# Kernel optimization log

Hardware: AMD Instinct MI355X
Metric: run time of the kernel (lower is better)

Reference implementation:

```python
import jax, jax.numpy as jnp
import numpy as np

LAMBDA_DEPTHG = 0.3
STEGO_TEMPERATURE = 0.1
KNN_K = 7
DEPTH_SIGMA = 0.5
EPS = 1e-8


def _l2norm(x):
    return x / jnp.sqrt(jnp.sum(x * x, axis=-1, keepdims=True) + EPS)


def _stego_loss(codes, feats, temperature, knn_k):
    # Pairwise cosine similarity of DINO features -> KNN graph (includes self).
    f = _l2norm(feats)                                  # (B,N,Df)
    sim_f = jnp.einsum('bnd,bmd->bnm', f, f)            # (B,N,N)
    _, knn_idx = jax.lax.top_k(sim_f, knn_k)            # (B,N,k) int32
    # Temperature-scaled InfoNCE over code similarities; KNN entries are positives.
    c = _l2norm(codes)                                  # (B,N,Dc)
    logits = jnp.einsum('bnd,bmd->bnm', c, c) / temperature  # (B,N,N)
    logp = jax.nn.log_softmax(logits, axis=-1)          # (B,N,N)
    pos_logp = jnp.take_along_axis(logp, knn_idx, axis=-1)   # (B,N,k)
    return -jnp.mean(pos_logp)


def _depth_guided_correlation_loss(codes, depth, sigma_d):
    # Gaussian depth affinity: pixels at similar depth should have similar codes.
    dd = depth[:, :, None] - depth[:, None, :]          # (B,N,N)
    w = jnp.exp(-(dd * dd) / (2.0 * sigma_d * sigma_d)) # (B,N,N)
    c = _l2norm(codes)
    s = jnp.einsum('bnd,bmd->bnm', c, c)                # (B,N,N) cosine corr
    return jnp.mean(w * (1.0 - s))


def setup_inputs() -> dict:
    key = jax.random.key(0)
    k1, k2, k3 = jax.random.split(key, 3)
    B, N = 2, 4096
    semantic_codes = jax.random.normal(k1, (B, N, 90), dtype=jnp.float32)
    dino_features = jax.random.normal(k2, (B, N, 384), dtype=jnp.float32)
    depth = jax.random.uniform(k3, (B, N), dtype=jnp.float32)
    return {"semantic_codes": semantic_codes, "dino_features": dino_features, "depth": depth}


def reference(semantic_codes, dino_features, depth):
    l_stego = _stego_loss(semantic_codes, dino_features, STEGO_TEMPERATURE, KNN_K)
    l_depthg = _depth_guided_correlation_loss(semantic_codes, depth, DEPTH_SIGMA)
    total = l_stego + LAMBDA_DEPTHG * l_depthg
    return (l_stego, l_depthg, total)
```

## Files before the change

kernel.cpp:

```cpp
#include <hip/hip_runtime.h>
#include <math.h>

#define NPTS 4096

typedef __attribute__((ext_vector_type(8))) short bf16x8;
typedef __attribute__((ext_vector_type(16))) float f32x16;
typedef long fp8x8;

#define KEEP(x) asm volatile("" : "+v"(x))

__device__ __forceinline__ f32x16 zero16() {
  f32x16 z;
#pragma unroll
  for (int i = 0; i < 16; ++i) z[i] = 0.f;
  return z;
}

__device__ __forceinline__ unsigned packkey(float x, int m) {
  unsigned u = __float_as_uint(x);
  unsigned key = u ^ ((unsigned)((int)u >> 31) | 0x80000000u);
  return (key & 0xFFFFF000u) | (unsigned)m;
}

__device__ __forceinline__ void cas7(unsigned v, unsigned* s) {
#pragma unroll
  for (int t = 0; t < 7; ++t) {
    const unsigned hi = s[t] >= v ? s[t] : v;
    const unsigned lo = s[t] >= v ? v : s[t];
    s[t] = hi;
    v = lo;
  }
}

#define KSENT 0u

__device__ __forceinline__ unsigned bf16pack(float a, float b) {
  unsigned ua = __float_as_uint(a); ua = (ua + 0x7FFFu + ((ua >> 16) & 1u)) >> 16;
  unsigned ub = __float_as_uint(b); ub = (ub + 0x7FFFu + ((ub >> 16) & 1u)) >> 16;
  return ua | (ub << 16);
}

__global__ __launch_bounds__(64) void norm_f(const float* __restrict__ feats,
                                             unsigned char* __restrict__ Fsw8) {
  const int row = blockIdx.x;
  const int lane = threadIdx.x;
  const int b = row >> 12, mt = (row >> 5) & 127, rl = row & 31;

  const float* f = feats + (size_t)row * 384;
  float v[8];
  float ss = 0.f;
  if (lane < 48) {
    float4 p0 = *(const float4*)(f + lane * 8);
    float4 p1 = *(const float4*)(f + lane * 8 + 4);
    v[0] = p0.x; v[1] = p0.y; v[2] = p0.z; v[3] = p0.w;
    v[4] = p1.x; v[5] = p1.y; v[6] = p1.z; v[7] = p1.w;
#pragma unroll
    for (int e = 0; e < 8; ++e) ss = fmaf(v[e], v[e], ss);
  }
#pragma unroll
  for (int m = 1; m <= 32; m <<= 1) ss += __shfl_xor(ss, m, 64);
  const float s8 = rsqrtf(ss + 1e-8f) * 8.0f;
  if (lane < 48) {
    int w0 = __builtin_amdgcn_cvt_pk_fp8_f32(v[0] * s8, v[1] * s8, 0, 0);
    w0 = __builtin_amdgcn_cvt_pk_fp8_f32(v[2] * s8, v[3] * s8, w0, 1);
    int w1 = __builtin_amdgcn_cvt_pk_fp8_f32(v[4] * s8, v[5] * s8, 0, 0);
    w1 = __builtin_amdgcn_cvt_pk_fp8_f32(v[6] * s8, v[7] * s8, w1, 1);
    const int kc = lane >> 1, hs = lane & 1;
    uint2 o = make_uint2((unsigned)w0, (unsigned)w1);
    *(uint2*)(Fsw8 + (((size_t)(b * 128 + mt) * 24 + kc) << 9) + (hs * 32 + rl) * 8) = o;
  }
}

__global__ __launch_bounds__(64) void norm_c(const float* __restrict__ codes,
                                             unsigned short* __restrict__ Csw,
                                             float* __restrict__ invc) {
  const int row = blockIdx.x;
  const int lane = threadIdx.x;
  const int b = row >> 12, mt = (row >> 5) & 127, rl = row & 31;

  const float* c = codes + (size_t)row * 90;
  float cv[8];
#pragma unroll
  for (int e = 0; e < 8; ++e) cv[e] = 0.f;
  if (lane < 11) {
    float4 p0 = *(const float4*)(c + lane * 8);
    float4 p1 = *(const float4*)(c + lane * 8 + 4);
    cv[0] = p0.x; cv[1] = p0.y; cv[2] = p0.z; cv[3] = p0.w;
    cv[4] = p1.x; cv[5] = p1.y; cv[6] = p1.z; cv[7] = p1.w;
  } else if (lane == 11) {
    cv[0] = c[88]; cv[1] = c[89];
  }
  float cs = 0.f;
#pragma unroll
  for (int e = 0; e < 8; ++e) cs = fmaf(cv[e], cv[e], cs);
#pragma unroll
  for (int m = 1; m <= 32; m <<= 1) cs += __shfl_xor(cs, m, 64);
  const float cinv = rsqrtf(cs + 1e-8f);
  if (lane < 12) {
    uint4 o;
    o.x = bf16pack(cv[0] * cinv, cv[1] * cinv);
    o.y = bf16pack(cv[2] * cinv, cv[3] * cinv);
    o.z = bf16pack(cv[4] * cinv, cv[5] * cinv);
    o.w = bf16pack(cv[6] * cinv, cv[7] * cinv);
    const int kc = lane >> 1, hs = lane & 1;
    *(uint4*)(Csw + (((size_t)(b * 128 + mt) * 6 + kc) << 9) + (hs * 32 + rl) * 8) = o;
  }
  if (lane == 0) invc[row] = cinv;
}

__global__ __launch_bounds__(256, 1) void knn_mfma(const unsigned char* __restrict__ Fsw8,
                                                   unsigned* __restrict__ cand) {
  __shared__ unsigned ckey[4][32][7];
  const int g = blockIdx.x;
  const int b = g & 1;
  const int p = (g >> 1) & 3;
  const int qt = g >> 3;
  const int q0 = qt * 32;
  const int tid = threadIdx.x;
  const int w = tid >> 6;
  const int lane = tid & 63;
  const int lo = lane & 31, hi4 = (lane >> 5) * 4;
  const unsigned char* Fb = Fsw8 + (size_t)b * 128 * 24 * 512;

  fp8x8 bfr[24];
  {
    const unsigned char* qb = Fb + ((size_t)qt * 24) * 512 + lane * 8;
#pragma unroll
    for (int t = 0; t < 24; ++t) bfr[t] = *(const fp8x8*)(qb + t * 512);
#pragma unroll
    for (int t = 0; t < 24; ++t) KEEP(bfr[t]);
  }
  unsigned s7[7];
#pragma unroll
  for (int t = 0; t < 7; ++t) s7[t] = KSENT;

  const int t0 = p * 32 + w * 8;
  const unsigned char* ab = Fb + ((size_t)t0 * 24) * 512 + lane * 8;

  fp8x8 a0[12], a1[12];
#pragma unroll
  for (int t = 0; t < 12; ++t) a0[t] = *(const fp8x8*)(ab + t * 512);
#pragma unroll
  for (int t = 0; t < 12; ++t) KEEP(a0[t]);

  for (int mt = 0; mt < 8; ++mt) {
    const unsigned char* art = ab + (size_t)mt * 24 * 512;
#pragma unroll
    for (int t = 0; t < 12; ++t) a1[t] = *(const fp8x8*)(art + (12 + t) * 512);
#pragma unroll
    for (int t = 0; t < 12; ++t) KEEP(a1[t]);
    f32x16 acc = zero16();
#pragma unroll
    for (int t = 0; t < 12; ++t)
      acc = __builtin_amdgcn_mfma_f32_32x32x16_fp8_fp8(a0[t], bfr[t], acc, 0, 0, 0);
    if (mt + 1 < 8) {
      const unsigned char* arn = ab + (size_t)(mt + 1) * 24 * 512;
#pragma unroll
      for (int t = 0; t < 12; ++t) a0[t] = *(const fp8x8*)(arn + t * 512);
#pragma unroll
      for (int t = 0; t < 12; ++t) KEEP(a0[t]);
    }
#pragma unroll
    for (int t = 0; t < 12; ++t)
      acc = __builtin_amdgcn_mfma_f32_32x32x16_fp8_fp8(a1[t], bfr[12 + t], acc, 0, 0, 0);
    const int mb = (t0 + mt) * 32 + hi4;
#pragma unroll
    for (int r = 0; r < 16; ++r) {
      const int m = mb + (r & 3) + 8 * (r >> 2);
      cas7(packkey(acc[r], m), s7);
    }
  }

#pragma unroll
  for (int t = 0; t < 7; ++t) {
    const unsigned ov = (unsigned)__shfl_xor((int)s7[t], 32, 64);
    cas7(ov, s7);
  }
  if (lane < 32) {
#pragma unroll
    for (int t = 0; t < 7; ++t) ckey[w][lo][t] = s7[t];
  }
  __syncthreads();

  if (tid < 32) {
    unsigned fs[7];
#pragma unroll
    for (int t = 0; t < 7; ++t) fs[t] = KSENT;
    for (int w2 = 0; w2 < 4; ++w2)
#pragma unroll
      for (int t = 0; t < 7; ++t) cas7(ckey[w2][tid][t], fs);
    unsigned* o = cand + ((size_t)((p * 2 + b) * NPTS) + q0 + tid) * 7;
#pragma unroll
    for (int t = 0; t < 7; ++t) o[t] = fs[t];
  }
}

__global__ __launch_bounds__(512, 1) void lse_depth(const unsigned short* __restrict__ Csw,
                                                    const float* __restrict__ depth,
                                                    float* __restrict__ slse_part,
                                                    float* __restrict__ dpart) {
  __shared__ float lsep[8][32];
  __shared__ float depp[8];
  const int g = blockIdx.x;
  const int b = g & 1;
  const int h = (g >> 1) & 1;
  const int qt = g >> 2;
  const int q0 = qt * 32;
  const int tid = threadIdx.x;
  const int w = tid >> 6;
  const int lane = tid & 63;
  const int lo = lane & 31, hi4 = (lane >> 5) * 4;
  const unsigned short* Cb = Csw + (size_t)b * 128 * 6 * 512;
  const float* db = depth + b * NPTS;

  bf16x8 bfr[6];
  {
    const unsigned short* qb = Cb + ((size_t)qt * 6) * 512 + lane * 8;
#pragma unroll
    for (int t = 0; t < 6; ++t) bfr[t] = *(const bf16x8*)(qb + t * 512);
#pragma unroll
    for (int t = 0; t < 6; ++t) KEEP(bfr[t]);
  }
  const float dq = db[q0 + lo];
  float slse = 0.f, sdep = 0.f;

  const int t0 = h * 64 + w * 8;
  const unsigned short* ab = Cb + ((size_t)t0 * 6) * 512 + lane * 8;

  bf16x8 a0[6], a1[6];
#pragma unroll
  for (int t = 0; t < 6; ++t) a0[t] = *(const bf16x8*)(ab + t * 512);
#pragma unroll
  for (int t = 0; t < 6; ++t) KEEP(a0[t]);

#define PROC3(A, GT)                                                           \
  {                                                                            \
    f32x16 acc = zero16();                                                     \
    _Pragma("unroll")                                                          \
    for (int t = 0; t < 6; ++t)                                                \
      acc = __builtin_amdgcn_mfma_f32_32x32x16_bf16(A[t], bfr[t], acc, 0, 0, 0); \
    float dvv[16];                                                             \
    _Pragma("unroll")                                                          \
    for (int k = 0; k < 4; ++k) {                                              \
      float4 dv = *(const float4*)(db + (GT) * 32 + hi4 + 8 * k);              \
      dvv[k * 4 + 0] = dv.x; dvv[k * 4 + 1] = dv.y;                            \
      dvv[k * 4 + 2] = dv.z; dvv[k * 4 + 3] = dv.w;                            \
    }                                                                          \
    _Pragma("unroll")                                                          \
    for (int r = 0; r < 16; ++r) {                                             \
      const float s = acc[r];                                                  \
      const float dd = dq - dvv[r];                                            \
      sdep += __expf(-2.f * dd * dd) * (1.f - s);                              \
      slse += __expf(fmaf(s, 10.f, -10.f));                                    \
    }                                                                          \
  }

  for (int mt = 0; mt < 8; mt += 2) {
    {
      const unsigned short* ar = ab + (size_t)(mt + 1) * 6 * 512;
#pragma unroll
      for (int t = 0; t < 6; ++t) a1[t] = *(const bf16x8*)(ar + t * 512);
#pragma unroll
      for (int t = 0; t < 6; ++t) KEEP(a1[t]);
    }
    PROC3(a0, t0 + mt)
    if (mt + 2 < 8) {
      const unsigned short* ar = ab + (size_t)(mt + 2) * 6 * 512;
#pragma unroll
      for (int t = 0; t < 6; ++t) a0[t] = *(const bf16x8*)(ar + t * 512);
#pragma unroll
      for (int t = 0; t < 6; ++t) KEEP(a0[t]);
    }
    PROC3(a1, t0 + mt + 1)
  }
#undef PROC3

  slse += __shfl_xor(slse, 32, 64);
  if (lane < 32) lsep[w][lo] = slse;
#pragma unroll
  for (int m = 1; m <= 32; m <<= 1) sdep += __shfl_xor(sdep, m, 64);
  if (lane == 0) depp[w] = sdep;
  __syncthreads();
  if (tid < 32) {
    float tot = 0.f;
#pragma unroll
    for (int w2 = 0; w2 < 8; ++w2) tot += lsep[w2][tid];
    slse_part[(size_t)((h * 2 + b) * NPTS) + q0 + tid] = tot;
  }
  if (tid == 32) {
    float d = 0.f;
#pragma unroll
    for (int w2 = 0; w2 < 8; ++w2) d += depp[w2];
    dpart[g] = d;
  }
}

__global__ __launch_bounds__(64) void gather_pos(const float* __restrict__ codes,
                                                 const float* __restrict__ invc,
                                                 const unsigned* __restrict__ cand,
                                                 float* __restrict__ gpart) {
  const int n = blockIdx.x;
  const int b = n >> 12, q = n & 4095;
  const int lane = threadIdx.x;

  unsigned s[7];
#pragma unroll
  for (int t = 0; t < 7; ++t) s[t] = KSENT;
#pragma unroll
  for (int pp = 0; pp < 4; ++pp) {
    const unsigned* cp = cand + ((size_t)((pp * 2 + b) * NPTS) + q) * 7;
#pragma unroll
    for (int t = 0; t < 7; ++t) cas7(cp[t], s);
  }
  bool has = false;
#pragma unroll
  for (int t = 0; t < 7; ++t) has = has || ((s[t] & 4095u) == (unsigned)q);
  if (!has) s[6] = (unsigned)q;

  const float* cn = codes + (size_t)n * 90;
  float2 a = make_float2(0.f, 0.f);
  if (lane < 45) a = *(const float2*)(cn + lane * 2);
  const float inva = invc[n];
  float ssum = 0.f;
#pragma unroll
  for (int k = 0; k < 7; ++k) {
    const int m = (int)(s[k] & 4095u);
    const float* cm = codes + ((size_t)(b << 12) + m) * 90;
    float2 bb = make_float2(0.f, 0.f);
    if (lane < 45) bb = *(const float2*)(cm + lane * 2);
    float p = fmaf(a.x, bb.x, a.y * bb.y);
#pragma unroll
    for (int w = 1; w <= 32; w <<= 1) p += __shfl_xor(p, w, 64);
    ssum += p * inva * invc[(b << 12) + m];
  }
  if (lane == 0) gpart[n] = ssum;
}

__global__ __launch_bounds__(256) void finalize(const float* __restrict__ slse_part,
                                                const float* __restrict__ gpart,
                                                const float* __restrict__ dpart,
                                                float* __restrict__ out) {
  const int tid = threadIdx.x;
  float s1 = 0.f, s2 = 0.f;
  for (int n = tid; n < 2 * NPTS; n += 256) {
    const int b = n >> 12, q = n & 4095;
    const float pz = slse_part[b * NPTS + q] + slse_part[(2 + b) * NPTS + q];
    s1 += 10.f + __logf(pz);
    s2 += gpart[n];
  }
  float s3 = dpart[tid] + dpart[tid + 256];
  __shared__ float r1[256], r2[256], r3[256];
  r1[tid] = s1; r2[tid] = s2; r3[tid] = s3;
  __syncthreads();
  for (int s = 128; s > 0; s >>= 1) {
    if (tid < s) { r1[tid] += r1[tid + s]; r2[tid] += r2[tid + s]; r3[tid] += r3[tid + s]; }
    __syncthreads();
  }
  if (tid == 0) {
    const float l_st = (7.f * r1[0] - 10.f * r2[0]) / 57344.f;
    const float l_dp = r3[0] / 33554432.f;
    out[0] = l_st;
    out[1] = l_dp;
    out[2] = l_st + 0.3f * l_dp;
  }
}

extern "C" void kernel_launch(void* const* d_in, const int* in_sizes, int n_in,
                              void* d_out, int out_size, void* d_ws, size_t ws_size,
                              hipStream_t stream) {
  (void)in_sizes; (void)n_in; (void)out_size; (void)ws_size;
  const float* codes = (const float*)d_in[0];
  const float* feats = (const float*)d_in[1];
  const float* depth = (const float*)d_in[2];
  float* out = (float*)d_out;

  char* ws = (char*)d_ws;
  float*    invc      = (float*)ws;
  unsigned* cand      = (unsigned*)(ws + 32768);
  unsigned char*  Fsw8 = (unsigned char*)(ws + 950272);
  unsigned short* Csw  = (unsigned short*)(ws + 950272);
  float*    slse_part = (float*)(ws + 2523136);
  float*    dpart     = (float*)(ws + 2654208);
  float*    gpart     = (float*)(ws + 2658304);

  norm_f<<<2 * NPTS, 64, 0, stream>>>(feats, Fsw8);
  knn_mfma<<<1024, 256, 0, stream>>>(Fsw8, cand);
  norm_c<<<2 * NPTS, 64, 0, stream>>>(codes, Csw, invc);
  lse_depth<<<512, 512, 0, stream>>>(Csw, depth, slse_part, dpart);
  gather_pos<<<2 * NPTS, 64, 0, stream>>>(codes, invc, cand, gpart);
  finalize<<<1, 256, 0, stream>>>(slse_part, gpart, dpart, out);
}
```

Measured before the change: 92.65 us.

## Fuse norm kernels and co-schedule KNN and LSE blocks in one launch

Merges the feature and code normalisation kernels into a single launch, and merges the KNN fp8 MFMA kernel and the LSE/depth bf16 MFMA kernel into one grid of 2048 blocks. Odd blocks do KNN and even blocks do LSE; the LSE work is repartitioned into four 256-thread slices per query tile, and finalize is updated to sum four partials. Csw now gets its own workspace region instead of aliasing Fsw8. This removes two launches and lets the compute-heavy KNN blocks overlap with the lighter LSE blocks on the GPU. The cost is register pressure from the union of both branches in one kernel and a changed LSE work split.

```diff
diff --git a/kernel.cpp b/kernel.cpp
--- a/kernel.cpp
+++ b/kernel.cpp
@@ -40,8 +40,11 @@
   return ua | (ub << 16);
 }
 
-__global__ __launch_bounds__(64) void norm_f(const float* __restrict__ feats,
-                                             unsigned char* __restrict__ Fsw8) {
+__global__ __launch_bounds__(64) void norm_all(const float* __restrict__ feats,
+                                               const float* __restrict__ codes,
+                                               unsigned char* __restrict__ Fsw8,
+                                               unsigned short* __restrict__ Csw,
+                                               float* __restrict__ invc) {
   const int row = blockIdx.x;
   const int lane = threadIdx.x;
   const int b = row >> 12, mt = (row >> 5) & 127, rl = row & 31;
@@ -69,14 +72,6 @@
     uint2 o = make_uint2((unsigned)w0, (unsigned)w1);
     *(uint2*)(Fsw8 + (((size_t)(b * 128 + mt) * 24 + kc) << 9) + (hs * 32 + rl) * 8) = o;
   }
-}
-
-__global__ __launch_bounds__(64) void norm_c(const float* __restrict__ codes,
-                                             unsigned short* __restrict__ Csw,
-                                             float* __restrict__ invc) {
-  const int row = blockIdx.x;
-  const int lane = threadIdx.x;
-  const int b = row >> 12, mt = (row >> 5) & 127, rl = row & 31;
 
   const float* c = codes + (size_t)row * 90;
   float cv[8];
@@ -108,10 +103,17 @@
   if (lane == 0) invc[row] = cinv;
 }
 
-__global__ __launch_bounds__(256, 1) void knn_mfma(const unsigned char* __restrict__ Fsw8,
-                                                   unsigned* __restrict__ cand) {
+__global__ __launch_bounds__(256, 1) void main_fused(const unsigned char* __restrict__ Fsw8,
+                                                     const unsigned short* __restrict__ Csw,
+                                                     const float* __restrict__ depth,
+                                                     unsigned* __restrict__ cand,
+                                                     float* __restrict__ slse_part,
+                                                     float* __restrict__ dpart) {
   __shared__ unsigned ckey[4][32][7];
-  const int g = blockIdx.x;
+  __shared__ float lsep[4][32];
+  __shared__ float depp[4];
+  const int gg = blockIdx.x;
+  const int g = gg >> 1;
   const int b = g & 1;
   const int p = (g >> 1) & 3;
   const int qt = g >> 3;
@@ -120,178 +122,161 @@
   const int w = tid >> 6;
   const int lane = tid & 63;
   const int lo = lane & 31, hi4 = (lane >> 5) * 4;
-  const unsigned char* Fb = Fsw8 + (size_t)b * 128 * 24 * 512;
-
-  fp8x8 bfr[24];
-  {
-    const unsigned char* qb = Fb + ((size_t)qt * 24) * 512 + lane * 8;
-#pragma unroll
-    for (int t = 0; t < 24; ++t) bfr[t] = *(const fp8x8*)(qb + t * 512);
-#pragma unroll
-    for (int t = 0; t < 24; ++t) KEEP(bfr[t]);
-  }
-  unsigned s7[7];
-#pragma unroll
-  for (int t = 0; t < 7; ++t) s7[t] = KSENT;
-
   const int t0 = p * 32 + w * 8;
-  const unsigned char* ab = Fb + ((size_t)t0 * 24) * 512 + lane * 8;
-
-  fp8x8 a0[12], a1[12];
-#pragma unroll
-  for (int t = 0; t < 12; ++t) a0[t] = *(const fp8x8*)(ab + t * 512);
-#pragma unroll
-  for (int t = 0; t < 12; ++t) KEEP(a0[t]);
-
-  for (int mt = 0; mt < 8; ++mt) {
-    const unsigned char* art = ab + (size_t)mt * 24 * 512;
-#pragma unroll
-    for (int t = 0; t < 12; ++t) a1[t] = *(const fp8x8*)(art + (12 + t) * 512);
-#pragma unroll
-    for (int t = 0; t < 12; ++t) KEEP(a1[t]);
-    f32x16 acc = zero16();
-#pragma unroll
-    for (int t = 0; t < 12; ++t)
-      acc = __builtin_amdgcn_mfma_f32_32x32x16_fp8_fp8(a0[t], bfr[t], acc, 0, 0, 0);
-    if (mt + 1 < 8) {
-      const unsigned char* arn = ab + (size_t)(mt + 1) * 24 * 512;
-#pragma unroll
-      for (int t = 0; t < 12; ++t) a0[t] = *(const fp8x8*)(arn + t * 512);
-#pragma unroll
-      for (int t = 0; t < 12; ++t) KEEP(a0[t]);
-    }
-#pragma unroll
-    for (int t = 0; t < 12; ++t)
-      acc = __builtin_amdgcn_mfma_f32_32x32x16_fp8_fp8(a1[t], bfr[12 + t], acc, 0, 0, 0);
-    const int mb = (t0 + mt) * 32 + hi4;
-#pragma unroll
-    for (int r = 0; r < 16; ++r) {
-      const int m = mb + (r & 3) + 8 * (r >> 2);
-      cas7(packkey(acc[r], m), s7);
-    }
-  }
-
-#pragma unroll
-  for (int t = 0; t < 7; ++t) {
-    const unsigned ov = (unsigned)__shfl_xor((int)s7[t], 32, 64);
-    cas7(ov, s7);
-  }
-  if (lane < 32) {
-#pragma unroll
-    for (int t = 0; t < 7; ++t) ckey[w][lo][t] = s7[t];
-  }
-  __syncthreads();
-
-  if (tid < 32) {
-    unsigned fs[7];
-#pragma unroll
-    for (int t = 0; t < 7; ++t) fs[t] = KSENT;
-    for (int w2 = 0; w2 < 4; ++w2)
-#pragma unroll
-      for (int t = 0; t < 7; ++t) cas7(ckey[w2][tid][t], fs);
-    unsigned* o = cand + ((size_t)((p * 2 + b) * NPTS) + q0 + tid) * 7;
-#pragma unroll
-    for (int t = 0; t < 7; ++t) o[t] = fs[t];
-  }
-}
-
-__global__ __launch_bounds__(512, 1) void lse_depth(const unsigned short* __restrict__ Csw,
-                                                    const float* __restrict__ depth,
-                                                    float* __restrict__ slse_part,
-                                                    float* __restrict__ dpart) {
-  __shared__ float lsep[8][32];
-  __shared__ float depp[8];
-  const int g = blockIdx.x;
-  const int b = g & 1;
-  const int h = (g >> 1) & 1;
-  const int qt = g >> 2;
-  const int q0 = qt * 32;
-  const int tid = threadIdx.x;
-  const int w = tid >> 6;
-  const int lane = tid & 63;
-  const int lo = lane & 31, hi4 = (lane >> 5) * 4;
-  const unsigned short* Cb = Csw + (size_t)b * 128 * 6 * 512;
-  const float* db = depth + b * NPTS;
-
-  bf16x8 bfr[6];
-  {
-    const unsigned short* qb = Cb + ((size_t)qt * 6) * 512 + lane * 8;
-#pragma unroll
-    for (int t = 0; t < 6; ++t) bfr[t] = *(const bf16x8*)(qb + t * 512);
-#pragma unroll
-    for (int t = 0; t < 6; ++t) KEEP(bfr[t]);
-  }
-  const float dq = db[q0 + lo];
-  float slse = 0.f, sdep = 0.f;
-
-  const int t0 = h * 64 + w * 8;
-  const unsigned short* ab = Cb + ((size_t)t0 * 6) * 512 + lane * 8;
-
-  bf16x8 a0[6], a1[6];
-#pragma unroll
-  for (int t = 0; t < 6; ++t) a0[t] = *(const bf16x8*)(ab + t * 512);
-#pragma unroll
-  for (int t = 0; t < 6; ++t) KEEP(a0[t]);
+
+  if (gg & 1) {
+    const unsigned char* Fb = Fsw8 + (size_t)b * 128 * 24 * 512;
+    fp8x8 bfr[24];
+    {
+      const unsigned char* qb = Fb + ((size_t)qt * 24) * 512 + lane * 8;
+#pragma unroll
+      for (int t = 0; t < 24; ++t) bfr[t] = *(const fp8x8*)(qb + t * 512);
+#pragma unroll
+      for (int t = 0; t < 24; ++t) KEEP(bfr[t]);
+    }
+    unsigned s7[7];
+#pragma unroll
+    for (int t = 0; t < 7; ++t) s7[t] = KSENT;
+
+    const unsigned char* ab = Fb + ((size_t)t0 * 24) * 512 + lane * 8;
+    fp8x8 a0[12], a1[12];
+#pragma unroll
+    for (int t = 0; t < 12; ++t) a0[t] = *(const fp8x8*)(ab + t * 512);
+#pragma unroll
+    for (int t = 0; t < 12; ++t) KEEP(a0[t]);
+
+    for (int mt = 0; mt < 8; ++mt) {
+      const unsigned char* art = ab + (size_t)mt * 24 * 512;
+#pragma unroll
+      for (int t = 0; t < 12; ++t) a1[t] = *(const fp8x8*)(art + (12 + t) * 512);
+#pragma unroll
+      for (int t = 0; t < 12; ++t) KEEP(a1[t]);
+      f32x16 acc = zero16();
+#pragma unroll
+      for (int t = 0; t < 12; ++t)
+        acc = __builtin_amdgcn_mfma_f32_32x32x16_fp8_fp8(a0[t], bfr[t], acc, 0, 0, 0);
+      if (mt + 1 < 8) {
+        const unsigned char* arn = ab + (size_t)(mt + 1) * 24 * 512;
+#pragma unroll
+        for (int t = 0; t < 12; ++t) a0[t] = *(const fp8x8*)(arn + t * 512);
+#pragma unroll
+        for (int t = 0; t < 12; ++t) KEEP(a0[t]);
+      }
+#pragma unroll
+      for (int t = 0; t < 12; ++t)
+        acc = __builtin_amdgcn_mfma_f32_32x32x16_fp8_fp8(a1[t], bfr[12 + t], acc, 0, 0, 0);
+      const int mb = (t0 + mt) * 32 + hi4;
+#pragma unroll
+      for (int r = 0; r < 16; ++r) {
+        const int m = mb + (r & 3) + 8 * (r >> 2);
+        cas7(packkey(acc[r], m), s7);
+      }
+    }
+
+#pragma unroll
+    for (int t = 0; t < 7; ++t) {
+      const unsigned ov = (unsigned)__shfl_xor((int)s7[t], 32, 64);
+      cas7(ov, s7);
+    }
+    if (lane < 32) {
+#pragma unroll
+      for (int t = 0; t < 7; ++t) ckey[w][lo][t] = s7[t];
+    }
+    __syncthreads();
+
+    if (tid < 32) {
+      unsigned fs[7];
+#pragma unroll
+      for (int t = 0; t < 7; ++t) fs[t] = KSENT;
+      for (int w2 = 0; w2 < 4; ++w2)
+#pragma unroll
+        for (int t = 0; t < 7; ++t) cas7(ckey[w2][tid][t], fs);
+      unsigned* o = cand + ((size_t)((p * 2 + b) * NPTS) + q0 + tid) * 7;
+#pragma unroll
+      for (int t = 0; t < 7; ++t) o[t] = fs[t];
+    }
+  } else {
+    const unsigned short* Cb = Csw + (size_t)b * 128 * 6 * 512;
+    const float* db = depth + b * NPTS;
+
+    bf16x8 bfr[6];
+    {
+      const unsigned short* qb = Cb + ((size_t)qt * 6) * 512 + lane * 8;
+#pragma unroll
+      for (int t = 0; t < 6; ++t) bfr[t] = *(const bf16x8*)(qb + t * 512);
+#pragma unroll
+      for (int t = 0; t < 6; ++t) KEEP(bfr[t]);
+    }
+    const float dq = db[q0 + lo];
+    float slse = 0.f, sdep = 0.f;
+
+    const unsigned short* ab = Cb + ((size_t)t0 * 6) * 512 + lane * 8;
+    bf16x8 a0[6], a1[6];
+#pragma unroll
+    for (int t = 0; t < 6; ++t) a0[t] = *(const bf16x8*)(ab + t * 512);
+#pragma unroll
+    for (int t = 0; t < 6; ++t) KEEP(a0[t]);
 
 #define PROC3(A, GT)                                                           \
-  {                                                                            \
-    f32x16 acc = zero16();                                                     \
-    _Pragma("unroll")                                                          \
-    for (int t = 0; t < 6; ++t)                                                \
-      acc = __builtin_amdgcn_mfma_f32_32x32x16_bf16(A[t], bfr[t], acc, 0, 0, 0); \
-    float dvv[16];                                                             \
-    _Pragma("unroll")                                                          \
-    for (int k = 0; k < 4; ++k) {                                              \
-      float4 dv = *(const float4*)(db + (GT) * 32 + hi4 + 8 * k);              \
-      dvv[k * 4 + 0] = dv.x; dvv[k * 4 + 1] = dv.y;                            \
-      dvv[k * 4 + 2] = dv.z; dvv[k * 4 + 3] = dv.w;                            \
-    }                                                                          \
-    _Pragma("unroll")                                                          \
-    for (int r = 0; r < 16; ++r) {                                             \
-      const float s = acc[r];                                                  \
-      const float dd = dq - dvv[r];                                            \
-      sdep += __expf(-2.f * dd * dd) * (1.f - s);                              \
-      slse += __expf(fmaf(s, 10.f, -10.f));                                    \
-    }                                                                          \
-  }
-
-  for (int mt = 0; mt < 8; mt += 2) {
-    {
-      const unsigned short* ar = ab + (size_t)(mt + 1) * 6 * 512;
-#pragma unroll
-      for (int t = 0; t < 6; ++t) a1[t] = *(const bf16x8*)(ar + t * 512);
-#pragma unroll
-      for (int t = 0; t < 6; ++t) KEEP(a1[t]);
-    }
-    PROC3(a0, t0 + mt)
-    if (mt + 2 < 8) {
-      const unsigned short* ar = ab + (size_t)(mt + 2) * 6 * 512;
-#pragma unroll
-      for (int t = 0; t < 6; ++t) a0[t] = *(const bf16x8*)(ar + t * 512);
-#pragma unroll
-      for (int t = 0; t < 6; ++t) KEEP(a0[t]);
-    }
-    PROC3(a1, t0 + mt + 1)
-  }
+    {                                                                          \
+      f32x16 acc = zero16();                                                   \
+      _Pragma("unroll")                                                        \
+      for (int t = 0; t < 6; ++t)                                              \
+        acc = __builtin_amdgcn_mfma_f32_32x32x16_bf16(A[t], bfr[t], acc, 0, 0, 0); \
+      float dvv[16];                                                           \
+      _Pragma("unroll")                                                        \
+      for (int k = 0; k < 4; ++k) {                                            \
+        float4 dv = *(const float4*)(db + (GT) * 32 + hi4 + 8 * k);            \
+        dvv[k * 4 + 0] = dv.x; dvv[k * 4 + 1] = dv.y;                          \
+        dvv[k * 4 + 2] = dv.z; dvv[k * 4 + 3] = dv.w;                          \
+      }                                                                        \
+      _Pragma("unroll")                                                        \
+      for (int r = 0; r < 16; ++r) {                                           \
+        const float s = acc[r];                                                \
+        const float dd = dq - dvv[r];                                          \
+        sdep += __expf(-2.f * dd * dd) * (1.f - s);                            \
+        slse += __expf(fmaf(s, 10.f, -10.f));                                  \
+      }                                                                        \
+    }
+
+    for (int mt = 0; mt < 8; mt += 2) {
+      {
+        const unsigned short* ar = ab + (size_t)(mt + 1) * 6 * 512;
+#pragma unroll
+        for (int t = 0; t < 6; ++t) a1[t] = *(const bf16x8*)(ar + t * 512);
+#pragma unroll
+        for (int t = 0; t < 6; ++t) KEEP(a1[t]);
+      }
+      PROC3(a0, t0 + mt)
+      if (mt + 2 < 8) {
+        const unsigned short* ar = ab + (size_t)(mt + 2) * 6 * 512;
+#pragma unroll
+        for (int t = 0; t < 6; ++t) a0[t] = *(const bf16x8*)(ar + t * 512);
+#pragma unroll
+        for (int t = 0; t < 6; ++t) KEEP(a0[t]);
+      }
+      PROC3(a1, t0 + mt + 1)
+    }
 #undef PROC3
 
-  slse += __shfl_xor(slse, 32, 64);
-  if (lane < 32) lsep[w][lo] = slse;
-#pragma unroll
-  for (int m = 1; m <= 32; m <<= 1) sdep += __shfl_xor(sdep, m, 64);
-  if (lane == 0) depp[w] = sdep;
-  __syncthreads();
-  if (tid < 32) {
-    float tot = 0.f;
-#pragma unroll
-    for (int w2 = 0; w2 < 8; ++w2) tot += lsep[w2][tid];
-    slse_part[(size_t)((h * 2 + b) * NPTS) + q0 + tid] = tot;
-  }
-  if (tid == 32) {
-    float d = 0.f;
-#pragma unroll
-    for (int w2 = 0; w2 < 8; ++w2) d += depp[w2];
-    dpart[g] = d;
+    slse += __shfl_xor(slse, 32, 64);
+    if (lane < 32) lsep[w][lo] = slse;
+#pragma unroll
+    for (int m = 1; m <= 32; m <<= 1) sdep += __shfl_xor(sdep, m, 64);
+    if (lane == 0) depp[w] = sdep;
+    __syncthreads();
+    if (tid < 32) {
+      float tot = 0.f;
+#pragma unroll
+      for (int w2 = 0; w2 < 4; ++w2) tot += lsep[w2][tid];
+      slse_part[(size_t)((p * 2 + b) * NPTS) + q0 + tid] = tot;
+    }
+    if (tid == 32) {
+      float d = 0.f;
+#pragma unroll
+      for (int w2 = 0; w2 < 4; ++w2) d += depp[w2];
+      dpart[g] = d;
+    }
   }
 }
 
@@ -344,11 +329,15 @@
   float s1 = 0.f, s2 = 0.f;
   for (int n = tid; n < 2 * NPTS; n += 256) {
     const int b = n >> 12, q = n & 4095;
-    const float pz = slse_part[b * NPTS + q] + slse_part[(2 + b) * NPTS + q];
+    float pz = 0.f;
+#pragma unroll
+    for (int pp = 0; pp < 4; ++pp) pz += slse_part[(pp * 2 + b) * NPTS + q];
     s1 += 10.f + __logf(pz);
     s2 += gpart[n];
   }
-  float s3 = dpart[tid] + dpart[tid + 256];
+  float s3 = 0.f;
+#pragma unroll
+  for (int k = 0; k < 4; ++k) s3 += dpart[tid + k * 256];
   __shared__ float r1[256], r2[256], r3[256];
   r1[tid] = s1; r2[tid] = s2; r3[tid] = s3;
   __syncthreads();
@@ -378,15 +367,13 @@
   float*    invc      = (float*)ws;
   unsigned* cand      = (unsigned*)(ws + 32768);
   unsigned char*  Fsw8 = (unsigned char*)(ws + 950272);
-  unsigned short* Csw  = (unsigned short*)(ws + 950272);
-  float*    slse_part = (float*)(ws + 2523136);
-  float*    dpart     = (float*)(ws + 2654208);
-  float*    gpart     = (float*)(ws + 2658304);
-
-  norm_f<<<2 * NPTS, 64, 0, stream>>>(feats, Fsw8);
-  knn_mfma<<<1024, 256, 0, stream>>>(Fsw8, cand);
-  norm_c<<<2 * NPTS, 64, 0, stream>>>(codes, Csw, invc);
-  lse_depth<<<512, 512, 0, stream>>>(Csw, depth, slse_part, dpart);
+  unsigned short* Csw  = (unsigned short*)(ws + 4096000);
+  float*    slse_part = (float*)(ws + 5668864);
+  float*    dpart     = (float*)(ws + 5799936);
+  float*    gpart     = (float*)(ws + 5804032);
+
+  norm_all<<<2 * NPTS, 64, 0, stream>>>(feats, codes, Fsw8, Csw, invc);
+  main_fused<<<2048, 256, 0, stream>>>(Fsw8, Csw, depth, cand, slse_part, dpart);
   gather_pos<<<2 * NPTS, 64, 0, stream>>>(codes, invc, cand, gpart);
   finalize<<<1, 256, 0, stream>>>(slse_part, gpart, dpart, out);
 }
```

New measurement: 99.11 us. 1.07x slower.

## Fuse normalization kernels and merge KNN partitions into single 1024-thread blocks

Applied to the files above, without the earlier changes.

Merges norm_f and norm_c into one kernel so a single launch writes the fp8 feature tiles, bf16 code tiles and inverse norms. Csw gets its own workspace region instead of aliasing Fsw8. The KNN kernel now uses 256 blocks of 1024 threads, each covering all key tiles for a query tile, so the 4-way candidate split and its merge in gather_pos go away. The A-operand double buffering is dropped in favour of a simpler load-then-compute sequence, which may expose more load latency, and the grid now has fewer blocks.

```diff
diff --git a/kernel.cpp b/kernel.cpp
--- a/kernel.cpp
+++ b/kernel.cpp
@@ -40,8 +40,11 @@
   return ua | (ub << 16);
 }
 
-__global__ __launch_bounds__(64) void norm_f(const float* __restrict__ feats,
-                                             unsigned char* __restrict__ Fsw8) {
+__global__ __launch_bounds__(64) void norm_all(const float* __restrict__ feats,
+                                               const float* __restrict__ codes,
+                                               unsigned char* __restrict__ Fsw8,
+                                               unsigned short* __restrict__ Csw,
+                                               float* __restrict__ invc) {
   const int row = blockIdx.x;
   const int lane = threadIdx.x;
   const int b = row >> 12, mt = (row >> 5) & 127, rl = row & 31;
@@ -69,14 +72,6 @@
     uint2 o = make_uint2((unsigned)w0, (unsigned)w1);
     *(uint2*)(Fsw8 + (((size_t)(b * 128 + mt) * 24 + kc) << 9) + (hs * 32 + rl) * 8) = o;
   }
-}
-
-__global__ __launch_bounds__(64) void norm_c(const float* __restrict__ codes,
-                                             unsigned short* __restrict__ Csw,
-                                             float* __restrict__ invc) {
-  const int row = blockIdx.x;
-  const int lane = threadIdx.x;
-  const int b = row >> 12, mt = (row >> 5) & 127, rl = row & 31;
 
   const float* c = codes + (size_t)row * 90;
   float cv[8];
@@ -108,13 +103,12 @@
   if (lane == 0) invc[row] = cinv;
 }
 
-__global__ __launch_bounds__(256, 1) void knn_mfma(const unsigned char* __restrict__ Fsw8,
-                                                   unsigned* __restrict__ cand) {
-  __shared__ unsigned ckey[4][32][7];
+__global__ __launch_bounds__(1024, 1) void knn_mfma(const unsigned char* __restrict__ Fsw8,
+                                                    unsigned* __restrict__ cand) {
+  __shared__ unsigned ckey[16][32][7];
   const int g = blockIdx.x;
   const int b = g & 1;
-  const int p = (g >> 1) & 3;
-  const int qt = g >> 3;
+  const int qt = g >> 1;
   const int q0 = qt * 32;
   const int tid = threadIdx.x;
   const int w = tid >> 6;
@@ -134,35 +128,27 @@
 #pragma unroll
   for (int t = 0; t < 7; ++t) s7[t] = KSENT;
 
-  const int t0 = p * 32 + w * 8;
+  const int t0 = w * 8;
   const unsigned char* ab = Fb + ((size_t)t0 * 24) * 512 + lane * 8;
 
-  fp8x8 a0[12], a1[12];
-#pragma unroll
-  for (int t = 0; t < 12; ++t) a0[t] = *(const fp8x8*)(ab + t * 512);
-#pragma unroll
-  for (int t = 0; t < 12; ++t) KEEP(a0[t]);
-
+  fp8x8 a[12];
   for (int mt = 0; mt < 8; ++mt) {
     const unsigned char* art = ab + (size_t)mt * 24 * 512;
-#pragma unroll
-    for (int t = 0; t < 12; ++t) a1[t] = *(const fp8x8*)(art + (12 + t) * 512);
-#pragma unroll
-    for (int t = 0; t < 12; ++t) KEEP(a1[t]);
     f32x16 acc = zero16();
 #pragma unroll
+    for (int t = 0; t < 12; ++t) a[t] = *(const fp8x8*)(art + t * 512);
+#pragma unroll
+    for (int t = 0; t < 12; ++t) KEEP(a[t]);
+#pragma unroll
     for (int t = 0; t < 12; ++t)
-      acc = __builtin_amdgcn_mfma_f32_32x32x16_fp8_fp8(a0[t], bfr[t], acc, 0, 0, 0);
-    if (mt + 1 < 8) {
-      const unsigned char* arn = ab + (size_t)(mt + 1) * 24 * 512;
-#pragma unroll
-      for (int t = 0; t < 12; ++t) a0[t] = *(const fp8x8*)(arn + t * 512);
-#pragma unroll
-      for (int t = 0; t < 12; ++t) KEEP(a0[t]);
-    }
+      acc = __builtin_amdgcn_mfma_f32_32x32x16_fp8_fp8(a[t], bfr[t], acc, 0, 0, 0);
+#pragma unroll
+    for (int t = 0; t < 12; ++t) a[t] = *(const fp8x8*)(art + (12 + t) * 512);
+#pragma unroll
+    for (int t = 0; t < 12; ++t) KEEP(a[t]);
 #pragma unroll
     for (int t = 0; t < 12; ++t)
-      acc = __builtin_amdgcn_mfma_f32_32x32x16_fp8_fp8(a1[t], bfr[12 + t], acc, 0, 0, 0);
+      acc = __builtin_amdgcn_mfma_f32_32x32x16_fp8_fp8(a[t], bfr[12 + t], acc, 0, 0, 0);
     const int mb = (t0 + mt) * 32 + hi4;
 #pragma unroll
     for (int r = 0; r < 16; ++r) {
@@ -186,10 +172,10 @@
     unsigned fs[7];
 #pragma unroll
     for (int t = 0; t < 7; ++t) fs[t] = KSENT;
-    for (int w2 = 0; w2 < 4; ++w2)
+    for (int w2 = 0; w2 < 16; ++w2)
 #pragma unroll
       for (int t = 0; t < 7; ++t) cas7(ckey[w2][tid][t], fs);
-    unsigned* o = cand + ((size_t)((p * 2 + b) * NPTS) + q0 + tid) * 7;
+    unsigned* o = cand + ((size_t)(b * NPTS) + q0 + tid) * 7;
 #pragma unroll
     for (int t = 0; t < 7; ++t) o[t] = fs[t];
   }
@@ -304,14 +290,9 @@
   const int lane = threadIdx.x;
 
   unsigned s[7];
-#pragma unroll
-  for (int t = 0; t < 7; ++t) s[t] = KSENT;
-#pragma unroll
-  for (int pp = 0; pp < 4; ++pp) {
-    const unsigned* cp = cand + ((size_t)((pp * 2 + b) * NPTS) + q) * 7;
-#pragma unroll
-    for (int t = 0; t < 7; ++t) cas7(cp[t], s);
-  }
+  const unsigned* cp = cand + (size_t)n * 7;
+#pragma unroll
+  for (int t = 0; t < 7; ++t) s[t] = cp[t];
   bool has = false;
 #pragma unroll
   for (int t = 0; t < 7; ++t) has = has || ((s[t] & 4095u) == (unsigned)q);
@@ -377,15 +358,14 @@
   char* ws = (char*)d_ws;
   float*    invc      = (float*)ws;
   unsigned* cand      = (unsigned*)(ws + 32768);
-  unsigned char*  Fsw8 = (unsigned char*)(ws + 950272);
-  unsigned short* Csw  = (unsigned short*)(ws + 950272);
-  float*    slse_part = (float*)(ws + 2523136);
-  float*    dpart     = (float*)(ws + 2654208);
-  float*    gpart     = (float*)(ws + 2658304);
-
-  norm_f<<<2 * NPTS, 64, 0, stream>>>(feats, Fsw8);
-  knn_mfma<<<1024, 256, 0, stream>>>(Fsw8, cand);
-  norm_c<<<2 * NPTS, 64, 0, stream>>>(codes, Csw, invc);
+  unsigned char*  Fsw8 = (unsigned char*)(ws + 262144);
+  unsigned short* Csw  = (unsigned short*)(ws + 3407872);
+  float*    slse_part = (float*)(ws + 4980736);
+  float*    dpart     = (float*)(ws + 5046272);
+  float*    gpart     = (float*)(ws + 5048320);
+
+  norm_all<<<2 * NPTS, 64, 0, stream>>>(feats, codes, Fsw8, Csw, invc);
+  knn_mfma<<<256, 1024, 0, stream>>>(Fsw8, cand);
   lse_depth<<<512, 512, 0, stream>>>(Csw, depth, slse_part, dpart);
   gather_pos<<<2 * NPTS, 64, 0, stream>>>(codes, invc, cand, gpart);
   finalize<<<1, 256, 0, stream>>>(slse_part, gpart, dpart, out);
```

Result: faster. 89.76 us (-3.1%).
